# Kernel tuning notes

Measured on AMD Instinct MI355X. Metric: run time of the kernel, lower is better.

Reference implementation:

```python
import jax, jax.numpy as jnp
import numpy as np


def setup_inputs() -> dict:
    key = jax.random.key(0)
    k1, k2, k3 = jax.random.split(key, 3)
    B, N, D = 4096, 8192, 1024
    protein_features = jax.random.normal(k1, (B, D), dtype=jnp.float32)
    function_features = jax.random.normal(k2, (N, D), dtype=jnp.float32)
    positive_mask = jax.random.randint(k3, (B, N), 0, 2, dtype=jnp.int32)
    temperature = jnp.zeros((1,), dtype=jnp.float32)  # exp(0) = 1
    return {
        "protein_features": protein_features,
        "function_features": function_features,
        "positive_mask": positive_mask,
        "temperature": temperature,
    }


def reference(protein_features, function_features, positive_mask, temperature):
    # logits: [B, N]
    logits = jnp.matmul(protein_features, function_features.T) / jnp.exp(temperature[0])
    # row-wise logsumexp, computed ONCE per row (the torch loop recomputes it per positive)
    lse = jax.nn.logsumexp(logits, axis=1, keepdims=True)  # [B, 1]
    m = (positive_mask == 1).astype(logits.dtype)          # [B, N]
    n_pos = m.sum()
    # per-pair loss = -pos_logit + logsumexp(row); mean over all positive pairs
    loss_sum = ((lse - logits) * m).sum()
    return jnp.where(n_pos > 0, loss_sum / n_pos, jnp.zeros((), dtype=logits.dtype))
```

## Files before the change

kernel.cpp:

```cpp
#include <hip/hip_runtime.h>
#include <hip/hip_bf16.h>

typedef __attribute__((ext_vector_type(4))) float f32x4;
typedef __attribute__((ext_vector_type(8))) __bf16 bf16x8;
typedef __attribute__((ext_vector_type(8))) unsigned short u16x8;

constexpr int BROWS = 4096;
constexpr int NCOLS = 8192;
constexpr int DK    = 1024;
constexpr int BM = 256, BN = 256, BK = 64;
constexpr int NCB = NCOLS / BN;
constexpr int NKT = DK / BK;
constexpr int NIT = NKT / 2;

__device__ static inline unsigned short f2bf(float f) {
  unsigned int u = __builtin_bit_cast(unsigned int, f);
  u += 0x7FFFu + ((u >> 16) & 1u);
  return (unsigned short)(u >> 16);
}

__device__ static inline void gload16(const void* g, void* l) {
  __builtin_amdgcn_global_load_lds(
      (const __attribute__((address_space(1))) void*)g,
      (__attribute__((address_space(3))) void*)l, 16, 0, 0);
}

__global__ void convert_kernel(const float* __restrict__ src,
                               unsigned short* __restrict__ dst,
                               int n4, int applyScale,
                               const float* __restrict__ temp) {
  float scale = applyScale ? expf(-temp[0]) : 1.0f;
  int i = blockIdx.x * blockDim.x + threadIdx.x;
  if (i >= n4) return;
  float4 v = reinterpret_cast<const float4*>(src)[i];
  ushort4 o;
  o.x = f2bf(v.x * scale);
  o.y = f2bf(v.y * scale);
  o.z = f2bf(v.z * scale);
  o.w = f2bf(v.w * scale);
  reinterpret_cast<ushort4*>(dst)[i] = o;
}

__device__ __forceinline__ void stage_half(const unsigned short* __restrict__ g,
                                           unsigned short* l, int t, int kt) {
#pragma unroll
  for (int p = 0; p < 2; ++p) {
    const int off = p * 8192 + t * 16;
    const int row = off >> 7;
    const int keSw = ((off & 127) >> 1) ^ ((row & 7) << 3);
    gload16(g + (size_t)row * DK + kt * 64 + keSw, l + (off >> 1));
  }
}

#define MFMA_BF16 __builtin_amdgcn_mfma_f32_16x16x32_bf16

#define LDS_FRAG(base, row, kk)                                             \
  __builtin_bit_cast(bf16x8, *reinterpret_cast<const u16x8*>(               \
      &(base)[((row) * 64 + (kk) * 32 + l4 * 8) ^ (((row) & 7) << 3)]))

#define READ_A(b, q)                                              \
  aFr[0][0] = LDS_FRAG(As[b][wm], (2*(q)    )*16 + l15, 0);       \
  aFr[0][1] = LDS_FRAG(As[b][wm], (2*(q)    )*16 + l15, 1);       \
  aFr[1][0] = LDS_FRAG(As[b][wm], (2*(q) + 1)*16 + l15, 0);       \
  aFr[1][1] = LDS_FRAG(As[b][wm], (2*(q) + 1)*16 + l15, 1);

#define READ_B(b)                                                 \
  bFr[0][0] = LDS_FRAG(Bs[b][bhB], brB +  0 + l15, 0);            \
  bFr[0][1] = LDS_FRAG(Bs[b][bhB], brB +  0 + l15, 1);            \
  bFr[1][0] = LDS_FRAG(Bs[b][bhB], brB + 16 + l15, 0);            \
  bFr[1][1] = LDS_FRAG(Bs[b][bhB], brB + 16 + l15, 1);            \
  bFr[2][0] = LDS_FRAG(Bs[b][bhB], brB + 32 + l15, 0);            \
  bFr[2][1] = LDS_FRAG(Bs[b][bhB], brB + 32 + l15, 1);            \
  bFr[3][0] = LDS_FRAG(Bs[b][bhB], brB + 48 + l15, 0);            \
  bFr[3][1] = LDS_FRAG(Bs[b][bhB], brB + 48 + l15, 1);

#define COMPUTE(q)                                                                  \
  __builtin_amdgcn_s_setprio(1);                                                   \
  _Pragma("unroll") for (int mm = 0; mm < 2; ++mm)                                  \
  _Pragma("unroll") for (int n = 0; n < 4; ++n) {                                   \
    acc[2*(q)+mm][n] = MFMA_BF16(aFr[mm][0], bFr[n][0], acc[2*(q)+mm][n], 0, 0, 0); \
    acc[2*(q)+mm][n] = MFMA_BF16(aFr[mm][1], bFr[n][1], acc[2*(q)+mm][n], 0, 0, 0); \
  }                                                                                 \
  __builtin_amdgcn_s_setprio(0);

#define PHASE_MID                                    \
  __builtin_amdgcn_s_barrier();                      \
  asm volatile("s_waitcnt lgkmcnt(0)" ::: "memory");

#define PHASE_END                                    \
  __builtin_amdgcn_s_barrier();

__global__ __launch_bounds__(512, 2)
void main_kernel(const unsigned short* __restrict__ Pb,
                 const unsigned short* __restrict__ Fb,
                 const int* __restrict__ mask,
                 f32x4* __restrict__ partials) {
  __shared__ __align__(16) unsigned short As[2][2][128 * 64];
  __shared__ __align__(16) unsigned short Bs[2][2][128 * 64];
  __shared__ unsigned long long maskBits[256 * 4];
  __shared__ float redM[4][256], redS[4][256], redP[4][256], redC[4][256];

  const int t    = threadIdx.x;
  const int lane = t & 63;
  const int w    = t >> 6;
  const int wm   = w >> 2;
  const int wn   = w & 3;
  const int l15  = lane & 15;
  const int l4   = lane >> 4;
  const int bhB  = wn >> 1;
  const int brB  = (wn & 1) * 64;

  const int brow = blockIdx.y * BM;
  const int bcol = blockIdx.x * BN;

  const unsigned short* Ag0 = Pb + (size_t)brow * DK;
  const unsigned short* Ag1 = Pb + (size_t)(brow + 128) * DK;
  const unsigned short* Bg0 = Fb + (size_t)bcol * DK;
  const unsigned short* Bg1 = Fb + (size_t)(bcol + 128) * DK;

  f32x4 acc[8][4] = {};
  bf16x8 bFr[4][2];
  bf16x8 aFr[2][2];

#pragma unroll
  for (int batch = 0; batch < 4; ++batch) {
    int v[32];
#pragma unroll
    for (int b = 0; b < 32; ++b) {
      const int g = w * 128 + batch * 32 + b;
      const int row = g >> 2, chunk = g & 3;
      v[b] = mask[(size_t)(brow + row) * NCOLS + bcol + chunk * 64 + lane];
    }
#pragma unroll
    for (int b = 0; b < 32; ++b) {
      const int g = w * 128 + batch * 32 + b;
      const int row = g >> 2, chunk = g & 3;
      unsigned long long bm = __ballot(v[b] == 1);
      if (lane == 0) maskBits[row * 4 + chunk] = bm;
    }
  }

  stage_half(Bg0, Bs[0][0], t, 0);
  stage_half(Bg1, Bs[0][1], t, 0);
  stage_half(Ag0, As[0][0], t, 0);
  stage_half(Ag1, As[0][1], t, 0);
  stage_half(Bg0, Bs[1][0], t, 1);
  stage_half(Bg1, Bs[1][1], t, 1);
  asm volatile("s_waitcnt vmcnt(4)" ::: "memory");
  __builtin_amdgcn_s_barrier();

  for (int i = 0; i < NIT; ++i) {
    const int t1 = 2 * i + 1;
    const bool more = (i < NIT - 1);
    READ_B(0); READ_A(0, 0);
    stage_half(Ag0, As[1][0], t, t1);
    PHASE_MID; COMPUTE(0); PHASE_END;
    READ_A(0, 1);
    stage_half(Ag1, As[1][1], t, t1);
    PHASE_MID; COMPUTE(1); PHASE_END;
    READ_A(0, 2);
    if (more) stage_half(Bg0, Bs[0][0], t, t1 + 1);
    PHASE_MID; COMPUTE(2); PHASE_END;
    READ_A(0, 3);
    if (more) stage_half(Bg1, Bs[0][1], t, t1 + 1);
    PHASE_MID; COMPUTE(3);
    if (more) { asm volatile("s_waitcnt vmcnt(4)" ::: "memory"); }
    else      { asm volatile("s_waitcnt vmcnt(0)" ::: "memory"); }
    PHASE_END;
    READ_B(1); READ_A(1, 0);
    if (more) stage_half(Ag0, As[0][0], t, t1 + 1);
    PHASE_MID; COMPUTE(0); PHASE_END;
    READ_A(1, 1);
    if (more) stage_half(Ag1, As[0][1], t, t1 + 1);
    PHASE_MID; COMPUTE(1); PHASE_END;
    READ_A(1, 2);
    if (more) stage_half(Bg0, Bs[1][0], t, t1 + 2);
    PHASE_MID; COMPUTE(2); PHASE_END;
    READ_A(1, 3);
    if (more) stage_half(Bg1, Bs[1][1], t, t1 + 2);
    PHASE_MID; COMPUTE(3);
    if (more) { asm volatile("s_waitcnt vmcnt(4)" ::: "memory"); }
    PHASE_END;
  }

#pragma unroll
  for (int m = 0; m < 8; ++m) {
#pragma unroll
    for (int r = 0; r < 4; ++r) {
      float v0 = acc[m][0][r], v1 = acc[m][1][r], v2 = acc[m][2][r], v3 = acc[m][3][r];
      float mx = fmaxf(fmaxf(v0, v1), fmaxf(v2, v3));
#pragma unroll
      for (int s = 1; s < 16; s <<= 1) mx = fmaxf(mx, __shfl_xor(mx, s, 64));
      float se = __expf(v0 - mx) + __expf(v1 - mx) + __expf(v2 - mx) + __expf(v3 - mx);

      const int lr = wm * 128 + m * 16 + l4 * 4 + r;
      const unsigned long long wB = maskBits[lr * 4 + wn];
      float ps = 0.f, pc = 0.f;
      if ((wB >> (l15     )) & 1ull) { ps += v0; pc += 1.f; }
      if ((wB >> (l15 + 16)) & 1ull) { ps += v1; pc += 1.f; }
      if ((wB >> (l15 + 32)) & 1ull) { ps += v2; pc += 1.f; }
      if ((wB >> (l15 + 48)) & 1ull) { ps += v3; pc += 1.f; }
#pragma unroll
      for (int s = 1; s < 16; s <<= 1) {
        se += __shfl_xor(se, s, 64);
        ps += __shfl_xor(ps, s, 64);
        pc += __shfl_xor(pc, s, 64);
      }
      if (l15 == 0) {
        redM[wn][lr] = mx;
        redS[wn][lr] = se;
        redP[wn][lr] = ps;
        redC[wn][lr] = pc;
      }
    }
  }
  __syncthreads();

  if (t < 256) {
    float m0 = redM[0][t], m1 = redM[1][t], m2 = redM[2][t], m3 = redM[3][t];
    float m  = fmaxf(fmaxf(m0, m1), fmaxf(m2, m3));
    float s  = redS[0][t] * __expf(m0 - m) + redS[1][t] * __expf(m1 - m)
             + redS[2][t] * __expf(m2 - m) + redS[3][t] * __expf(m3 - m);
    float ps = redP[0][t] + redP[1][t] + redP[2][t] + redP[3][t];
    float pc = redC[0][t] + redC[1][t] + redC[2][t] + redC[3][t];
    f32x4 out4;
    out4.x = m; out4.y = s; out4.z = ps; out4.w = pc;
    partials[(size_t)(brow + t) * NCB + blockIdx.x] = out4;
  }
}

__global__ void row_reduce_kernel(const f32x4* __restrict__ partials,
                                  float* __restrict__ rowContrib,
                                  float* __restrict__ rowCnt) {
  const int row  = blockIdx.x * 4 + (threadIdx.x >> 6);
  const int lane = threadIdx.x & 63;
  f32x4 p = partials[(size_t)row * NCB + (lane & 31)];
  float m = p.x;
#pragma unroll
  for (int s = 1; s < 32; s <<= 1) m = fmaxf(m, __shfl_xor(m, s, 64));
  float se = p.y * __expf(p.x - m);
  float ps = p.z, pc = p.w;
#pragma unroll
  for (int s = 1; s < 32; s <<= 1) {
    se += __shfl_xor(se, s, 64);
    ps += __shfl_xor(ps, s, 64);
    pc += __shfl_xor(pc, s, 64);
  }
  if (lane == 0) {
    float lse = m + logf(se);
    rowContrib[row] = pc * lse - ps;
    rowCnt[row]     = pc;
  }
}

__global__ void final_kernel(const float* __restrict__ rowContrib,
                             const float* __restrict__ rowCnt,
                             float* __restrict__ out) {
  __shared__ double sC[256];
  __shared__ double sN[256];
  double c = 0.0, n = 0.0;
  for (int i = threadIdx.x; i < BROWS; i += 256) {
    c += (double)rowContrib[i];
    n += (double)rowCnt[i];
  }
  sC[threadIdx.x] = c;
  sN[threadIdx.x] = n;
  __syncthreads();
  for (int s = 128; s > 0; s >>= 1) {
    if ((int)threadIdx.x < s) {
      sC[threadIdx.x] += sC[threadIdx.x + s];
      sN[threadIdx.x] += sN[threadIdx.x + s];
    }
    __syncthreads();
  }
  if (threadIdx.x == 0) out[0] = (sN[0] > 0.0) ? (float)(sC[0] / sN[0]) : 0.0f;
}

extern "C" void kernel_launch(void* const* d_in, const int* in_sizes, int n_in,
                              void* d_out, int out_size, void* d_ws, size_t ws_size,
                              hipStream_t stream) {
  const float* P    = (const float*)d_in[0];
  const float* F    = (const float*)d_in[1];
  const int*   mask = (const int*)d_in[2];
  const float* temp = (const float*)d_in[3];
  float* out = (float*)d_out;

  char* ws = (char*)d_ws;
  unsigned short* Pb = (unsigned short*)ws;
  unsigned short* Fb = (unsigned short*)(ws + (size_t)BROWS * DK * 2);
  f32x4* partials    = (f32x4*)(ws + (size_t)(BROWS + NCOLS) * DK * 2);
  float* rowContrib  = (float*)((char*)partials + (size_t)BROWS * NCB * sizeof(f32x4));
  float* rowCnt      = rowContrib + BROWS;

  const int nP4 = BROWS * DK / 4;
  const int nF4 = NCOLS * DK / 4;
  hipLaunchKernelGGL(convert_kernel, dim3(nP4 / 256), dim3(256), 0, stream, P, Pb, nP4, 1, temp);
  hipLaunchKernelGGL(convert_kernel, dim3(nF4 / 256), dim3(256), 0, stream, F, Fb, nF4, 0, temp);
  hipLaunchKernelGGL(main_kernel, dim3(NCOLS / BN, BROWS / BM), dim3(512), 0, stream, Pb, Fb, mask, partials);
  hipLaunchKernelGGL(row_reduce_kernel, dim3(BROWS / 4), dim3(256), 0, stream, partials, rowContrib, rowCnt);
  hipLaunchKernelGGL(final_kernel, dim3(1), dim3(256), 0, stream, rowContrib, rowCnt, out);
}
```

Measured before the change: 132.0 us.

## Pack positive mask into bitmask in a separate kernel before the GEMM

Moves the int32 mask-to-bitmask ballot packing out of the GEMM block prologue into a standalone streaming kernel that writes a global 64-bit-word bitmask. The GEMM epilogue then reads mask words directly from global memory, and the per-block LDS mask buffer and its prologue loads go away. The intent is to stop each GEMM block stalling on a large mask tile load before its matmul pipeline starts, and to free LDS. In exchange it adds a kernel launch, a workspace bitmask, and scattered global loads in the epilogue.

```diff
diff --git a/kernel.cpp b/kernel.cpp
--- a/kernel.cpp
+++ b/kernel.cpp
@@ -12,6 +12,7 @@
 constexpr int NCB = NCOLS / BN;
 constexpr int NKT = DK / BK;
 constexpr int NIT = NKT / 2;
+constexpr int NWRDS = BROWS * NCOLS / 64;
 
 __device__ static inline unsigned short f2bf(float f) {
   unsigned int u = __builtin_bit_cast(unsigned int, f);
@@ -41,6 +42,24 @@
   reinterpret_cast<ushort4*>(dst)[i] = o;
 }
 
+__global__ void maskpack_kernel(const int* __restrict__ mask,
+                                unsigned long long* __restrict__ bits) {
+  const int lane = threadIdx.x & 63;
+  const int gw   = (blockIdx.x * blockDim.x + threadIdx.x) >> 6;
+  const int nw   = (gridDim.x * blockDim.x) >> 6;
+  for (int base = gw * 8; base < NWRDS; base += nw * 8) {
+    int v[8];
+#pragma unroll
+    for (int j = 0; j < 8; ++j)
+      v[j] = mask[(size_t)(base + j) * 64 + lane];
+#pragma unroll
+    for (int j = 0; j < 8; ++j) {
+      unsigned long long bm = __ballot(v[j] == 1);
+      if (lane == 0) bits[base + j] = bm;
+    }
+  }
+}
+
 __device__ __forceinline__ void stage_half(const unsigned short* __restrict__ g,
                                            unsigned short* l, int t, int kt) {
 #pragma unroll
@@ -93,11 +112,10 @@
 __global__ __launch_bounds__(512, 2)
 void main_kernel(const unsigned short* __restrict__ Pb,
                  const unsigned short* __restrict__ Fb,
-                 const int* __restrict__ mask,
+                 const unsigned long long* __restrict__ bits,
                  f32x4* __restrict__ partials) {
   __shared__ __align__(16) unsigned short As[2][2][128 * 64];
   __shared__ __align__(16) unsigned short Bs[2][2][128 * 64];
-  __shared__ unsigned long long maskBits[256 * 4];
   __shared__ float redM[4][256], redS[4][256], redP[4][256], redC[4][256];
 
   const int t    = threadIdx.x;
@@ -121,24 +139,6 @@
   f32x4 acc[8][4] = {};
   bf16x8 bFr[4][2];
   bf16x8 aFr[2][2];
-
-#pragma unroll
-  for (int batch = 0; batch < 4; ++batch) {
-    int v[32];
-#pragma unroll
-    for (int b = 0; b < 32; ++b) {
-      const int g = w * 128 + batch * 32 + b;
-      const int row = g >> 2, chunk = g & 3;
-      v[b] = mask[(size_t)(brow + row) * NCOLS + bcol + chunk * 64 + lane];
-    }
-#pragma unroll
-    for (int b = 0; b < 32; ++b) {
-      const int g = w * 128 + batch * 32 + b;
-      const int row = g >> 2, chunk = g & 3;
-      unsigned long long bm = __ballot(v[b] == 1);
-      if (lane == 0) maskBits[row * 4 + chunk] = bm;
-    }
-  }
 
   stage_half(Bg0, Bs[0][0], t, 0);
   stage_half(Bg1, Bs[0][1], t, 0);
@@ -194,7 +194,8 @@
       float se = __expf(v0 - mx) + __expf(v1 - mx) + __expf(v2 - mx) + __expf(v3 - mx);
 
       const int lr = wm * 128 + m * 16 + l4 * 4 + r;
-      const unsigned long long wB = maskBits[lr * 4 + wn];
+      const unsigned long long wB =
+          bits[(size_t)(brow + lr) * (NCOLS / 64) + (bcol >> 6) + wn];
       float ps = 0.f, pc = 0.f;
       if ((wB >> (l15     )) & 1ull) { ps += v0; pc += 1.f; }
       if ((wB >> (l15 + 16)) & 1ull) { ps += v1; pc += 1.f; }
@@ -288,7 +289,8 @@
   char* ws = (char*)d_ws;
   unsigned short* Pb = (unsigned short*)ws;
   unsigned short* Fb = (unsigned short*)(ws + (size_t)BROWS * DK * 2);
-  f32x4* partials    = (f32x4*)(ws + (size_t)(BROWS + NCOLS) * DK * 2);
+  unsigned long long* bits = (unsigned long long*)(ws + (size_t)(BROWS + NCOLS) * DK * 2);
+  f32x4* partials    = (f32x4*)((char*)bits + (size_t)NWRDS * 8);
   float* rowContrib  = (float*)((char*)partials + (size_t)BROWS * NCB * sizeof(f32x4));
   float* rowCnt      = rowContrib + BROWS;
 
@@ -296,7 +298,8 @@
   const int nF4 = NCOLS * DK / 4;
   hipLaunchKernelGGL(convert_kernel, dim3(nP4 / 256), dim3(256), 0, stream, P, Pb, nP4, 1, temp);
   hipLaunchKernelGGL(convert_kernel, dim3(nF4 / 256), dim3(256), 0, stream, F, Fb, nF4, 0, temp);
-  hipLaunchKernelGGL(main_kernel, dim3(NCOLS / BN, BROWS / BM), dim3(512), 0, stream, Pb, Fb, mask, partials);
+  hipLaunchKernelGGL(maskpack_kernel, dim3(2048), dim3(256), 0, stream, mask, bits);
+  hipLaunchKernelGGL(main_kernel, dim3(NCOLS / BN, BROWS / BM), dim3(512), 0, stream, Pb, Fb, bits, partials);
   hipLaunchKernelGGL(row_reduce_kernel, dim3(BROWS / 4), dim3(256), 0, stream, partials, rowContrib, rowCnt);
   hipLaunchKernelGGL(final_kernel, dim3(1), dim3(256), 0, stream, rowContrib, rowCnt, out);
 }
```

After: 139.7 us. +5.8%, slower.
